# Kernel tuning notes

Hardware: AMD Instinct MI355X
Metric: run time of the kernel (lower is better)

Reference implementation:

```python
import jax, jax.numpy as jnp
import numpy as np

V, E, H, T = 50000, 128, 256, 9
H2 = H // 2
B, S = 128, 512


def setup_inputs() -> dict:
    key = jax.random.key(0)
    ks = jax.random.split(key, 12)
    sc = 0.05
    return {
        "x": jax.random.randint(ks[0], (B, S), 0, V, dtype=jnp.int64) if False else jax.random.randint(ks[0], (B, S), 0, V).astype(jnp.int64),
        "mask": jnp.ones((B, S), dtype=jnp.int32),
        "embed": jax.random.normal(ks[1], (V, E), jnp.float32) * sc,
        "W_ih_f": jax.random.normal(ks[2], (4 * H2, E), jnp.float32) * sc,
        "W_hh_f": jax.random.normal(ks[3], (4 * H2, H2), jnp.float32) * sc,
        "b_f": jax.random.normal(ks[4], (4 * H2,), jnp.float32) * sc,
        "W_ih_b": jax.random.normal(ks[5], (4 * H2, E), jnp.float32) * sc,
        "W_hh_b": jax.random.normal(ks[6], (4 * H2, H2), jnp.float32) * sc,
        "b_b": jax.random.normal(ks[7], (4 * H2,), jnp.float32) * sc,
        "W_out": jax.random.normal(ks[8], (T, H), jnp.float32) * sc,
        "b_out": jax.random.normal(ks[9], (T,), jnp.float32) * sc,
        "start_trans": jax.random.normal(ks[10], (T,), jnp.float32) * sc,
        "trans": jax.random.normal(ks[11], (T, T), jnp.float32) * sc,
        "end_trans": jax.random.normal(jax.random.fold_in(key, 99), (T,), jnp.float32) * sc,
    }


def _lstm_dir(xg, W_hh, reverse):
    # xg: [B,S,4*H2] precomputed input projections (+bias)
    if reverse:
        xg = xg[:, ::-1]
    b = xg.shape[0]
    h0 = jnp.zeros((b, H2), xg.dtype)

    def step(carry, xt):
        h, c = carry
        g = xt + h @ W_hh.T
        i, f, gg, o = jnp.split(g, 4, axis=-1)
        c = jax.nn.sigmoid(f) * c + jax.nn.sigmoid(i) * jnp.tanh(gg)
        h = jax.nn.sigmoid(o) * jnp.tanh(c)
        return (h, c), h

    _, hs = jax.lax.scan(step, (h0, h0), jnp.swapaxes(xg, 0, 1))
    hs = jnp.swapaxes(hs, 0, 1)  # [B,S,H2]
    if reverse:
        hs = hs[:, ::-1]
    return hs


def _emissions(x, embed, W_ih_f, W_hh_f, b_f, W_ih_b, W_hh_b, b_b, W_out, b_out):
    emb = embed[x]  # [B,S,E]
    xg_f = jnp.einsum('bse,ge->bsg', emb, W_ih_f) + b_f
    xg_b = jnp.einsum('bse,ge->bsg', emb, W_ih_b) + b_b
    h_f = _lstm_dir(xg_f, W_hh_f, False)
    h_b = _lstm_dir(xg_b, W_hh_b, True)
    feats = jnp.concatenate([h_f, h_b], axis=-1)  # [B,S,H]
    return jnp.einsum('bsh,th->bst', feats, W_out) + b_out  # [B,S,T]


def _viterbi(emissions, mask, start_trans, trans, end_trans):
    # emissions [B,S,T], mask [B,S] (1 = valid prefix)
    m = mask.astype(bool)
    score0 = start_trans + emissions[:, 0]  # [B,T]

    def fwd_step(score, inp):
        em_t, m_t = inp  # [B,T], [B]
        nxt = score[:, :, None] + trans[None] + em_t[:, None, :]  # [B,prev,next]
        best = nxt.max(axis=1)
        idx = nxt.argmax(axis=1).astype(jnp.int32)  # [B,T] backpointers
        score = jnp.where(m_t[:, None], best, score)
        return score, idx

    em_rest = jnp.swapaxes(emissions[:, 1:], 0, 1)  # [S-1,B,T]
    m_rest = jnp.swapaxes(m[:, 1:], 0, 1)  # [S-1,B]
    score, history = jax.lax.scan(fwd_step, score0, (em_rest, m_rest))
    final = score + end_trans
    best_scores = final.max(axis=-1)  # [B]
    cur = final.argmax(axis=-1).astype(jnp.int32)  # [B] tag at last valid step

    def back_step(cur, inp):
        hist_t, m_t = inp  # [B,T], [B]
        tag = jnp.where(m_t, cur, -1)  # -1 pads positions beyond seq end
        prev = jnp.take_along_axis(hist_t, cur[:, None], axis=1)[:, 0]
        cur = jnp.where(m_t, prev, cur)
        return cur, tag

    cur0, tags_rev = jax.lax.scan(back_step, cur, (history[::-1], m_rest[::-1]))
    paths = jnp.concatenate(
        [cur0[:, None], jnp.swapaxes(tags_rev, 0, 1)[:, ::-1]], axis=1)  # [B,S]
    return paths, best_scores


def reference(x, mask, embed, W_ih_f, W_hh_f, b_f, W_ih_b, W_hh_b, b_b,
              W_out, b_out, start_trans, trans, end_trans):
    emissions = _emissions(x, embed, W_ih_f, W_hh_f, b_f,
                           W_ih_b, W_hh_b, b_b, W_out, b_out)
    paths, best_scores = _viterbi(emissions, mask, start_trans, trans, end_trans)
    return paths, best_scores
```

## Files before the change

kernel.cpp:

```cpp
#include <hip/hip_runtime.h>
#include <stdint.h>

#define S_LEN 512
#define NT 9

typedef __attribute__((ext_vector_type(8)))  short          bf16x8;
typedef __attribute__((ext_vector_type(4)))  float          f32x4;
typedef __attribute__((ext_vector_type(4)))  unsigned short u16x4;

static __device__ __forceinline__ unsigned short f2bf(float f) {
    union { float f; unsigned u; } c; c.f = f;
    return (unsigned short)((c.u + 0x7fffu + ((c.u >> 16) & 1u)) >> 16);
}
static __device__ __forceinline__ float bf2f(unsigned short h) {
    union { unsigned u; float f; } c; c.u = ((unsigned)h) << 16;
    return c.f;
}
static __device__ __forceinline__ bf16x8 cvt8(const float* p) {
    f32x4 a = *(const f32x4*)p, b = *(const f32x4*)(p + 4);
    bf16x8 fr;
    fr[0]=(short)f2bf(a[0]); fr[1]=(short)f2bf(a[1]); fr[2]=(short)f2bf(a[2]); fr[3]=(short)f2bf(a[3]);
    fr[4]=(short)f2bf(b[0]); fr[5]=(short)f2bf(b[1]); fr[6]=(short)f2bf(b[2]); fr[7]=(short)f2bf(b[3]);
    return fr;
}
static __device__ __forceinline__ float sigf(float x) {
    return __builtin_amdgcn_rcpf(1.0f + __expf(-x));
}
static __device__ __forceinline__ float tanhf_(float x) {
    return 1.0f - 2.0f * __builtin_amdgcn_rcpf(1.0f + __expf(2.0f * x));
}

static __device__ __forceinline__ void wg_barrier_lds() {
    asm volatile("s_waitcnt lgkmcnt(0)" ::: "memory");
    __builtin_amdgcn_s_barrier();
    asm volatile("" ::: "memory");
}

__global__ __launch_bounds__(256) void k_ebf(
    const float* __restrict__ embed, unsigned short* __restrict__ ebf)
{
    const size_t n4 = 1600000;
    for (size_t i = blockIdx.x * 256 + threadIdx.x; i < n4; i += (size_t)2048 * 256) {
        f32x4 v = *(const f32x4*)(embed + i * 4);
        u16x4 o;
        o[0] = f2bf(v[0]); o[1] = f2bf(v[1]); o[2] = f2bf(v[2]); o[3] = f2bf(v[3]);
        *(u16x4*)(ebf + i * 4) = o;
    }
}

__global__ __launch_bounds__(512) void k_lstm(
    const unsigned short* __restrict__ ebf, const int* __restrict__ x,
    const float* __restrict__ Whf, const float* __restrict__ Whb,
    const float* __restrict__ Wif, const float* __restrict__ Wib,
    const float* __restrict__ bF,  const float* __restrict__ bB,
    unsigned short* __restrict__ feats)
{
    const int dir = blockIdx.y, bt = blockIdx.x;
    const float* __restrict__ Wh   = dir ? Whb : Whf;
    const float* __restrict__ Wi   = dir ? Wib : Wif;
    const float* __restrict__ bias = dir ? bB  : bF;
    const int tid = threadIdx.x, w = tid >> 6, L = tid & 63, l15 = L & 15, l4 = L >> 4;

    bf16x8 Bh[4][4], Bi[4][4];
    float  bq[4];
#pragma unroll
    for (int q = 0; q < 4; ++q) {
        const int gate = q * 128 + w * 16 + l15;
        bq[q] = bias[gate];
#pragma unroll
        for (int kt = 0; kt < 4; ++kt) {
            Bh[q][kt] = cvt8(Wh + gate * 128 + kt * 32 + l4 * 8);
            Bi[q][kt] = cvt8(Wi + gate * 128 + kt * 32 + l4 * 8);
        }
    }

    __shared__ unsigned short hl[2048];
    for (int i = tid; i < 1024; i += 512) ((unsigned*)hl)[i] = 0;

    const int ar = l15 >> 2;
    int rdoff[4];
#pragma unroll
    for (int kt = 0; kt < 4; ++kt) {
        int p = (kt * 4 + l4 + 2 * ar) & 15;
        rdoff[kt] = ar * 256 + p * 16;
    }
    const int hc = w * 16 + l15;
    const int wroff = l4 * 256 + (((hc >> 3) + 2 * l4) & 15) * 16 + (hc & 7) * 2;

    float c = 0.f;
    const int* __restrict__ xrowA = x + (bt * 4 + ar) * S_LEN;
    unsigned short* fcur = feats + ((size_t)(bt * 4 + l4) * 512 + (dir ? 511 : 0)) * 256
                                 + dir * 128 + hc;
    const ptrdiff_t fstep = dir ? -256 : 256;

    bf16x8 eA[4], eB[4];
    {
        const int tok0 = xrowA[dir ? 511 : 0];
        const unsigned short* eb = ebf + (size_t)tok0 * 128 + l4 * 8;
#pragma unroll
        for (int kt = 0; kt < 4; ++kt) eA[kt] = *(const bf16x8*)(eb + kt * 32);
    }
    int tkN = xrowA[dir ? 510 : 1];

    f32x4 acc[4];
#pragma unroll
    for (int q = 0; q < 4; ++q) acc[q] = f32x4{0.f, 0.f, 0.f, 0.f};

    __syncthreads();

#define LSTM_STEP(T, EC, EN)                                                    \
    {                                                                           \
        const int t_ = (T);                                                     \
        const char* bufR = (const char*)hl + (t_ & 1) * 1024;                   \
        char*       bufW = (char*)hl + ((t_ & 1) ^ 1) * 1024;                   \
                         \
        const int t2_ = (t_ < 510) ? (t_ + 2) : 511;                            \
        int tknew = xrowA[dir ? (511 - t2_) : t2_];                             \
              \
        const unsigned short* eb_ = ebf + (size_t)tkN * 128 + l4 * 8;           \
        _Pragma("unroll")                                                       \
        for (int kt = 0; kt < 4; ++kt) EN[kt] = *(const bf16x8*)(eb_ + kt * 32);\
                                                                \
        bf16x8 A_[4];                                                           \
        _Pragma("unroll")                                                       \
        for (int kt = 0; kt < 4; ++kt)                                          \
            A_[kt] = *(const bf16x8*)(bufR + rdoff[kt]);                        \
          \
        _Pragma("unroll")                                                       \
        for (int q = 0; q < 4; ++q) {                                           \
            acc[q][0] = bq[q];                                                  \
            _Pragma("unroll")                                                   \
            for (int kt = 0; kt < 4; ++kt)                                      \
                acc[q] = __builtin_amdgcn_mfma_f32_16x16x32_bf16(               \
                             EC[kt], Bi[q][kt], acc[q], 0, 0, 0);               \
            _Pragma("unroll")                                                   \
            for (int kt = 0; kt < 4; ++kt)                                      \
                acc[q] = __builtin_amdgcn_mfma_f32_16x16x32_bf16(               \
                             A_[kt], Bh[q][kt], acc[q], 0, 0, 0);               \
        }                                                                       \
        float ig = sigf(acc[0][0]);                                             \
        float fg = sigf(acc[1][0]);                                             \
        float gg = tanhf_(acc[2][0]);                                           \
        float og = sigf(acc[3][0]);                                             \
        c = fg * c + ig * gg;                                                   \
        float h_ = og * tanhf_(c);                                              \
        unsigned short hb = f2bf(h_);                                           \
        *(unsigned short*)(bufW + wroff) = hb;                                  \
        *fcur = hb; fcur += fstep;                                              \
        wg_barrier_lds();                                                       \
        tkN = tknew;                                                            \
    }

    for (int it = 0; it < 256; ++it) {
        LSTM_STEP(2 * it,     eA, eB)
        LSTM_STEP(2 * it + 1, eB, eA)
    }
#undef LSTM_STEP
}

__global__ __launch_bounds__(256) void k_viterbi(
    const unsigned short* __restrict__ feats, const float* __restrict__ Wout,
    const int* __restrict__ mask, const float* __restrict__ bout,
    const float* __restrict__ startt, const float* __restrict__ trans,
    const float* __restrict__ endt, float* __restrict__ out)
{
    const int b = blockIdx.x, tid = threadIdx.x;
    const int w = tid >> 6, L = tid & 63, l15 = L & 15, l4 = L >> 4;
    __shared__ float em[512 * 9];
    __shared__ int   msk[512];
    __shared__ unsigned char hist[512 * 9];
    __shared__ unsigned char Gl[32 * 12];
    __shared__ unsigned char bound[32];
    __shared__ int curS;

    bf16x8 Of[2][4];
#pragma unroll
    for (int d = 0; d < 2; ++d)
#pragma unroll
        for (int kt = 0; kt < 4; ++kt) { bf16x8 z;
#pragma unroll
            for (int i = 0; i < 8; ++i) z[i] = 0; Of[d][kt] = z; }
    float bv = 0.f;
    if (l15 < NT) {
        bv = bout[l15];
#pragma unroll
        for (int d = 0; d < 2; ++d)
#pragma unroll
            for (int kt = 0; kt < 4; ++kt)
                Of[d][kt] = cvt8(Wout + l15 * 256 + d * 128 + kt * 32 + l4 * 8);
    }

    for (int i = tid; i < 512; i += 256) msk[i] = mask[b * 512 + i];

#pragma unroll
    for (int i = 0; i < 8; ++i) {
        const int sg = w * 8 + i;
        const unsigned short* frow = feats + ((size_t)b * 512 + sg * 16 + l15) * 256;
        f32x4 e0 = {0, 0, 0, 0}, e1 = {0, 0, 0, 0};
#pragma unroll
        for (int kt = 0; kt < 4; ++kt) {
            bf16x8 A = *(const bf16x8*)(frow + kt * 32 + l4 * 8);
            e0 = __builtin_amdgcn_mfma_f32_16x16x32_bf16(A, Of[0][kt], e0, 0, 0, 0);
        }
#pragma unroll
        for (int kt = 0; kt < 4; ++kt) {
            bf16x8 A = *(const bf16x8*)(frow + 128 + kt * 32 + l4 * 8);
            e1 = __builtin_amdgcn_mfma_f32_16x16x32_bf16(A, Of[1][kt], e1, 0, 0, 0);
        }
        if (l15 < NT) {
#pragma unroll
            for (int j = 0; j < 4; ++j)
                em[(sg * 16 + l4 * 4 + j) * 9 + l15] = (e0[j] + e1[j]) + bv;
        }
    }
    __syncthreads();

    if (tid < 64) {
        const int k = (tid < NT) ? tid : 0;
        float trk[9];
#pragma unroll
        for (int j = 0; j < NT; ++j) trk[j] = trans[j * 9 + k];
        float score = startt[k] + em[k];
        for (int t = 1; t < 512; ++t) {
            float v[9];
#pragma unroll
            for (int j = 0; j < NT; ++j) v[j] = __shfl(score, j, 64) + trk[j];
            float m01 = fmaxf(v[0], v[1]), m23 = fmaxf(v[2], v[3]);
            float m45 = fmaxf(v[4], v[5]), m67 = fmaxf(v[6], v[7]);
            float m = fmaxf(fmaxf(fmaxf(m01, m23), fmaxf(m45, m67)), v[8]);
            int bi = 0;
#pragma unroll
            for (int j = 8; j >= 0; --j) if (v[j] == m) bi = j;
            if (msk[t]) score = m + em[t * 9 + k];
            if (tid < NT) hist[t * 9 + tid] = (unsigned char)bi;
        }
        float fin = score + endt[k];
        float bs = -3e38f; int cur = 0;
#pragma unroll
        for (int j = 0; j < NT; ++j) {
            float vv = __shfl(fin, j, 64);
            if (vv > bs) { bs = vv; cur = j; }
        }
        if (tid == 0) { curS = cur; out[65536 + b] = bs; }
    }
    __syncthreads();

    if (tid < 32) {
        const int m = tid;
        int G[9];
#pragma unroll
        for (int k = 0; k < NT; ++k) G[k] = k;
        const int hi = (m == 31) ? 511 : (16 * m + 16);
        for (int t = hi; t >= 16 * m + 1; --t) {
            if (msk[t]) {
#pragma unroll
                for (int k = 0; k < NT; ++k) G[k] = hist[t * 9 + G[k]];
            }
        }
#pragma unroll
        for (int k = 0; k < NT; ++k) Gl[m * 12 + k] = (unsigned char)G[k];
    }
    __syncthreads();

    if (tid == 0) {
        int e = curS;
        bound[31] = (unsigned char)e;
        for (int m = 31; m >= 1; --m) { e = Gl[m * 12 + e]; bound[m - 1] = (unsigned char)e; }
        out[(size_t)b * 512] = (float)Gl[0 * 12 + e];
    }
    __syncthreads();

    if (tid < 32) {
        const int m = tid;
        int ccur = bound[m];
        const int hi = (m == 31) ? 511 : (16 * m + 16);
        for (int t = hi; t >= 16 * m + 1; --t) {
            const int mt = msk[t];
            out[(size_t)b * 512 + t] = (float)(mt ? ccur : -1);
            if (mt) ccur = hist[t * 9 + ccur];
        }
    }
}

extern "C" void kernel_launch(void* const* d_in, const int* in_sizes, int n_in,
                              void* d_out, int out_size, void* d_ws, size_t ws_size,
                              hipStream_t stream) {
    const int*   x      = (const int*)d_in[0];
    const int*   mask   = (const int*)d_in[1];
    const float* embed  = (const float*)d_in[2];
    const float* Wihf   = (const float*)d_in[3];
    const float* Whhf   = (const float*)d_in[4];
    const float* bf_    = (const float*)d_in[5];
    const float* Wihb   = (const float*)d_in[6];
    const float* Whhb   = (const float*)d_in[7];
    const float* bb_    = (const float*)d_in[8];
    const float* Wout   = (const float*)d_in[9];
    const float* bout   = (const float*)d_in[10];
    const float* startt = (const float*)d_in[11];
    const float* trans  = (const float*)d_in[12];
    const float* endt   = (const float*)d_in[13];

    unsigned short* ebf   = (unsigned short*)d_ws;
    unsigned short* feats = (unsigned short*)((char*)d_ws + (size_t)16777216);
    float*          out   = (float*)d_out;

    k_ebf    <<<2048,        256, 0, stream>>>(embed, ebf);
    k_lstm   <<<dim3(32, 2), 512, 0, stream>>>(ebf, x, Whhf, Whhb, Wihf, Wihb, bf_, bb_, feats);
    k_viterbi<<<128,         256, 0, stream>>>(feats, Wout, mask, bout, startt, trans, endt, out);
}
```

Before: 507.6 us.

## Batch input projection MFMAs over four timesteps per chunk in LSTM loop

Reorganizes the recurrent LSTM loop so the input-projection MFMAs (embedding times W_ih) are computed once per group of four timesteps. Each MFMA row now carries a different timestep instead of a different batch element. This removes 16 of the 32 MFMAs from each serial step's critical path, leaving only the recurrent h·W_hh product inside the step. It relies on a remapped embedding-row layout (row = batch*4 + time offset) and adds an extra batched MFMA block every four steps.

```diff
diff --git a/kernel.cpp b/kernel.cpp
--- a/kernel.cpp
+++ b/kernel.cpp
@@ -87,73 +87,85 @@
     const int hc = w * 16 + l15;
     const int wroff = l4 * 256 + (((hc >> 3) + 2 * l4) & 15) * 16 + (hc & 7) * 2;
 
-    float c = 0.f;
-    const int* __restrict__ xrowA = x + (bt * 4 + ar) * S_LEN;
+    float cst = 0.f;
+    const int* __restrict__ xrowA = x + (bt * 4 + (l15 >> 2)) * S_LEN;
+    const int soff = l15 & 3;
     unsigned short* fcur = feats + ((size_t)(bt * 4 + l4) * 512 + (dir ? 511 : 0)) * 256
                                  + dir * 128 + hc;
     const ptrdiff_t fstep = dir ? -256 : 256;
 
-    bf16x8 eA[4], eB[4];
+    bf16x8 embA[4];
     {
-        const int tok0 = xrowA[dir ? 511 : 0];
+        const int t0_ = soff;
+        const int tok0 = xrowA[dir ? (511 - t0_) : t0_];
         const unsigned short* eb = ebf + (size_t)tok0 * 128 + l4 * 8;
 #pragma unroll
-        for (int kt = 0; kt < 4; ++kt) eA[kt] = *(const bf16x8*)(eb + kt * 32);
-    }
-    int tkN = xrowA[dir ? 510 : 1];
-
-    f32x4 acc[4];
-#pragma unroll
-    for (int q = 0; q < 4; ++q) acc[q] = f32x4{0.f, 0.f, 0.f, 0.f};
-
-    __syncthreads();
-
-#define LSTM_STEP(T, EC, EN)                                                    \
+        for (int kt = 0; kt < 4; ++kt) embA[kt] = *(const bf16x8*)(eb + kt * 32);
+    }
+    int tokN;
+    {
+        const int t1_ = 4 + soff;
+        tokN = xrowA[dir ? (511 - t1_) : t1_];
+    }
+
+    f32x4 gacc[4];
+#pragma unroll
+    for (int q = 0; q < 4; ++q) gacc[q] = f32x4{0.f, 0.f, 0.f, 0.f};
+
+    __syncthreads();
+
+#define LSTM_STEP(J)                                                            \
     {                                                                           \
-        const int t_ = (T);                                                     \
-        const char* bufR = (const char*)hl + (t_ & 1) * 1024;                   \
-        char*       bufW = (char*)hl + ((t_ & 1) ^ 1) * 1024;                   \
-                         \
-        const int t2_ = (t_ < 510) ? (t_ + 2) : 511;                            \
-        int tknew = xrowA[dir ? (511 - t2_) : t2_];                             \
-              \
-        const unsigned short* eb_ = ebf + (size_t)tkN * 128 + l4 * 8;           \
-        _Pragma("unroll")                                                       \
-        for (int kt = 0; kt < 4; ++kt) EN[kt] = *(const bf16x8*)(eb_ + kt * 32);\
-                                                                \
+        const char* bufR = (const char*)hl + ((J) & 1) * 1024;                  \
+        char*       bufW = (char*)hl + ((((J) & 1)) ^ 1) * 1024;                \
         bf16x8 A_[4];                                                           \
         _Pragma("unroll")                                                       \
         for (int kt = 0; kt < 4; ++kt)                                          \
             A_[kt] = *(const bf16x8*)(bufR + rdoff[kt]);                        \
-          \
         _Pragma("unroll")                                                       \
-        for (int q = 0; q < 4; ++q) {                                           \
-            acc[q][0] = bq[q];                                                  \
+        for (int q = 0; q < 4; ++q) gacc[q][0] = xa[q][(J)];                    \
+        _Pragma("unroll")                                                       \
+        for (int kt = 0; kt < 4; ++kt)                                          \
             _Pragma("unroll")                                                   \
-            for (int kt = 0; kt < 4; ++kt)                                      \
-                acc[q] = __builtin_amdgcn_mfma_f32_16x16x32_bf16(               \
-                             EC[kt], Bi[q][kt], acc[q], 0, 0, 0);               \
-            _Pragma("unroll")                                                   \
-            for (int kt = 0; kt < 4; ++kt)                                      \
-                acc[q] = __builtin_amdgcn_mfma_f32_16x16x32_bf16(               \
-                             A_[kt], Bh[q][kt], acc[q], 0, 0, 0);               \
-        }                                                                       \
-        float ig = sigf(acc[0][0]);                                             \
-        float fg = sigf(acc[1][0]);                                             \
-        float gg = tanhf_(acc[2][0]);                                           \
-        float og = sigf(acc[3][0]);                                             \
-        c = fg * c + ig * gg;                                                   \
-        float h_ = og * tanhf_(c);                                              \
+            for (int q = 0; q < 4; ++q)                                         \
+                gacc[q] = __builtin_amdgcn_mfma_f32_16x16x32_bf16(              \
+                              A_[kt], Bh[q][kt], gacc[q], 0, 0, 0);             \
+        float ig = sigf(gacc[0][0]);                                            \
+        float fg = sigf(gacc[1][0]);                                            \
+        float gg = tanhf_(gacc[2][0]);                                          \
+        float og = sigf(gacc[3][0]);                                            \
+        cst = fg * cst + ig * gg;                                               \
+        float h_ = og * tanhf_(cst);                                            \
         unsigned short hb = f2bf(h_);                                           \
         *(unsigned short*)(bufW + wroff) = hb;                                  \
         *fcur = hb; fcur += fstep;                                              \
         wg_barrier_lds();                                                       \
-        tkN = tknew;                                                            \
-    }
-
-    for (int it = 0; it < 256; ++it) {
-        LSTM_STEP(2 * it,     eA, eB)
-        LSTM_STEP(2 * it + 1, eB, eA)
+    }
+
+    for (int cc = 0; cc < 128; ++cc) {
+        f32x4 xa[4];
+#pragma unroll
+        for (int q = 0; q < 4; ++q) xa[q] = f32x4{ bq[q], bq[q], bq[q], bq[q] };
+#pragma unroll
+        for (int kt = 0; kt < 4; ++kt)
+#pragma unroll
+            for (int q = 0; q < 4; ++q)
+                xa[q] = __builtin_amdgcn_mfma_f32_16x16x32_bf16(
+                            embA[kt], Bi[q][kt], xa[q], 0, 0, 0);
+        {
+            const unsigned short* eb = ebf + (size_t)tokN * 128 + l4 * 8;
+#pragma unroll
+            for (int kt = 0; kt < 4; ++kt) embA[kt] = *(const bf16x8*)(eb + kt * 32);
+        }
+        {
+            int tc2 = 4 * (cc + 2) + soff;
+            tc2 = (tc2 > 511) ? 511 : tc2;
+            tokN = xrowA[dir ? (511 - tc2) : tc2];
+        }
+        LSTM_STEP(0)
+        LSTM_STEP(1)
+        LSTM_STEP(2)
+        LSTM_STEP(3)
     }
 #undef LSTM_STEP
 }
```

Result: faster. 432.8 us (-14.7%).
